# Kernel tuning notes

Measured on AMD Instinct MI355X. Metric: run time of the kernel, lower is better.

The kernel has to match this reference:

```python
import jax, jax.numpy as jnp
import numpy as np

D_IN = 128
HID = 32
HEADS = 8
OUT = 16
N = 50000
E = 400000
NEG_SLOPE = 0.2


def setup_inputs() -> dict:
    key = jax.random.key(0)
    ks = jax.random.split(key, 12)
    s = lambda k, sh: jax.random.normal(k, sh, dtype=jnp.float32) * 0.05
    return {
        "x": jax.random.normal(ks[0], (N, D_IN), dtype=jnp.float32),
        "edge_index": jax.random.randint(ks[1], (2, E), 0, N, dtype=jnp.int64),
        # conv_1: GATv2, heads=8, concat=True
        "W1l": s(ks[2], (D_IN, HEADS * HID)),
        "W1r": s(ks[3], (D_IN, HEADS * HID)),
        "att1": s(ks[4], (HEADS, HID)),
        "b1": jnp.zeros((HEADS * HID,), dtype=jnp.float32),
        # conv_2: GATv2, heads=1, concat=False
        "W2l": s(ks[5], (HEADS * HID, HID)),
        "W2r": s(ks[6], (HEADS * HID, HID)),
        "att2": s(ks[7], (1, HID)),
        "b2": jnp.zeros((HID,), dtype=jnp.float32),
        # final linear
        "Wlin": s(ks[8], (HID, OUT)),
        "blin": jnp.zeros((OUT,), dtype=jnp.float32),
    }


def _gatv2(x, src, dst, Wl, Wr, att, bias, n_nodes):
    heads, ch = att.shape
    xl = (x @ Wl).reshape(n_nodes, heads, ch)   # source-side transform
    xr = (x @ Wr).reshape(n_nodes, heads, ch)   # target-side transform
    # per-edge GATv2 score: a^T leaky_relu(xl_i + xr_j)
    e = jax.nn.leaky_relu(xl[src] + xr[dst], NEG_SLOPE)        # [E,H,C]
    logits = jnp.einsum('ehc,hc->eh', e, att)                  # [E,H]
    # segment softmax grouped by destination node
    m = jax.ops.segment_max(logits, dst, num_segments=n_nodes)
    m = jnp.where(jnp.isfinite(m), m, 0.0)
    p = jnp.exp(logits - m[dst])
    denom = jax.ops.segment_sum(p, dst, num_segments=n_nodes)
    alpha = p / jnp.maximum(denom[dst], 1e-16)                 # [E,H]
    # scatter-sum aggregation of weighted source features
    out = jax.ops.segment_sum(alpha[:, :, None] * xl[src], dst, num_segments=n_nodes)
    return out + bias.reshape(1, heads, ch)                    # [N,H,C]


def reference(x, edge_index, W1l, W1r, att1, b1, W2l, W2r, att2, b2, Wlin, blin):
    n = x.shape[0]
    loops = jnp.arange(n, dtype=edge_index.dtype)
    ei = jnp.concatenate([edge_index, jnp.stack([loops, loops])], axis=1)  # add_self_loops=True
    src, dst = ei[0], ei[1]

    h = _gatv2(x, src, dst, W1l, W1r, att1, b1, n)   # [N,8,32]
    h = jax.nn.elu(h.reshape(n, -1))                  # concat=True; dropout=identity (eval)

    h = _gatv2(h, src, dst, W2l, W2r, att2, b2, n)   # [N,1,32]
    h = jax.nn.elu(h[:, 0, :])                        # concat=False, heads=1 -> mean == squeeze

    return h @ Wlin + blin                            # [N,16]
```

## Files before the change

### kernel.cpp

```cpp
#include <hip/hip_runtime.h>
#include <cstdint>
#include <cstddef>

#define N_NODES 50000
#define N_EDGES 400000
#define E_TOT   (N_EDGES + N_NODES)
#define D_INF   128
#define C1      256
#define HIDC    32
#define OUTC    16
#define NEG_SLOPE 0.2f
#define LOG2E   1.44269504088896340736f

#define ESRC_CAP (E_TOT + 3 * N_NODES + 16)

#define ZB_DEG ((N_NODES + 255) / 256)
#define TB_W   ((2 * D_INF * C1 + 2 * C1 * HIDC + 255) / 256)
#define PREP_GRID (ZB_DEG + TB_W + 1)

#define GB1   ((((N_NODES + 31) / 32) + 3) / 4)
#define DEGB  ((E_TOT + 255) / 256)
#define FILLB ((E_TOT + 255) / 256)

typedef __bf16 bf16x8 __attribute__((ext_vector_type(8)));
typedef float  floatx4 __attribute__((ext_vector_type(4)));
typedef float  floatx2 __attribute__((ext_vector_type(2)));
typedef int    intx4  __attribute__((ext_vector_type(4)));
typedef unsigned int uintx4 __attribute__((ext_vector_type(4)));
typedef unsigned int uintx2 __attribute__((ext_vector_type(2)));
typedef unsigned short ushortx8 __attribute__((ext_vector_type(8)));
typedef unsigned short ushortx4 __attribute__((ext_vector_type(4)));

__device__ __forceinline__ unsigned short f2bf(float f) {
  unsigned int u = __builtin_bit_cast(unsigned int, f);
  u += 0x7FFFu + ((u >> 16) & 1u);
  return (unsigned short)(u >> 16);
}
__device__ __forceinline__ float bf2f(unsigned short u) {
  return __builtin_bit_cast(float, (unsigned int)u << 16);
}
__device__ __forceinline__ floatx2 bf2x2(unsigned int u) {
  floatx2 r;
  r.x = __builtin_bit_cast(float, u << 16);
  r.y = __builtin_bit_cast(float, u & 0xffff0000u);
  return r;
}

__device__ __forceinline__ int ld_src(const int* ei, int f, int e) {
  return f ? ei[2 * e] : ei[e];
}
__device__ __forceinline__ int ld_dst(const int* ei, int f, int e) {
  return f ? ei[2 * (N_EDGES + e)] : ei[N_EDGES + e];
}

__global__ __launch_bounds__(256) void k_prep(
    const int* __restrict__ ei,
    const float* __restrict__ W1l, const float* __restrict__ W1r,
    const float* __restrict__ W2l, const float* __restrict__ W2r,
    unsigned short* __restrict__ W1lT, unsigned short* __restrict__ W1rT,
    unsigned short* __restrict__ W2lT, unsigned short* __restrict__ W2rT,
    int* __restrict__ deg, int* __restrict__ total, int* __restrict__ flag) {
  __shared__ int sdet;
  const int bid = blockIdx.x;
  const int tid = threadIdx.x;
  if (bid < ZB_DEG) {
    const int i = bid * 256 + tid;
    if (i < N_NODES) deg[i] = 0;
    if (bid == 0 && tid == 0) *total = 0;
    return;
  }
  if (bid < ZB_DEG + TB_W) {
    int idx = (bid - ZB_DEG) * 256 + tid;
    if (idx < D_INF * C1) {
      const int r = idx >> 8, c = idx & 255;
      W1lT[c * D_INF + r] = f2bf(W1l[idx]);
    } else if (idx < 2 * D_INF * C1) {
      idx -= D_INF * C1;
      const int r = idx >> 8, c = idx & 255;
      W1rT[c * D_INF + r] = f2bf(W1r[idx]);
    } else if (idx < 2 * D_INF * C1 + C1 * HIDC) {
      idx -= 2 * D_INF * C1;
      const int r = idx >> 5, c = idx & 31;
      W2lT[c * C1 + r] = f2bf(W2l[idx]);
    } else {
      idx -= 2 * D_INF * C1 + C1 * HIDC;
      const int r = idx >> 5, c = idx & 31;
      W2rT[c * C1 + r] = f2bf(W2r[idx]);
    }
    return;
  }
  if (tid == 0) sdet = 0;
  __syncthreads();
  if (tid < 64) atomicOr(&sdet, ei[2 * tid + 1]);
  __syncthreads();
  if (tid == 0) *flag = (sdet == 0) ? 1 : 0;
}

__global__ __launch_bounds__(256) void k_alloc(
    const int* __restrict__ deg, int* __restrict__ rowptr,
    int* __restrict__ cursor, int* __restrict__ total) {
  const int i = blockIdx.x * 256 + threadIdx.x;
  const int lane = threadIdx.x & 63;
  const int d  = (i < N_NODES) ? deg[i] : 0;
  const int d4 = (d + 3) & ~3;
  int incl = d4;
#pragma unroll
  for (int off = 1; off < 64; off <<= 1) {
    int t = __shfl_up(incl, off);
    if (lane >= off) incl += t;
  }
  const int wtot = __shfl(incl, 63);
  int wb = 0;
  if (lane == 63) wb = atomicAdd(total, wtot);
  wb = __shfl(wb, 63);
  if (i < N_NODES) {
    const int e = wb + incl - d4;
    rowptr[i] = e;
    cursor[i] = e;
  }
}

__global__ void k_fill(const int* __restrict__ ei, const int* __restrict__ flag,
                       int* __restrict__ cursor, int* __restrict__ esrc) {
  int e = blockIdx.x * 256 + threadIdx.x;
  if (e < E_TOT) {
    int src, dst;
    if (e < N_EDGES) { src = ld_src(ei, *flag, e); dst = ld_dst(ei, *flag, e); }
    else             { src = dst = e - N_EDGES; }
    if ((unsigned)src < N_NODES && (unsigned)dst < N_NODES) {
      int pos = atomicAdd(&cursor[dst], 1);
      esrc[pos] = src;
    }
  }
}

__device__ __forceinline__ bf16x8 load8(const unsigned short* p) {
  uintx4 raw = *reinterpret_cast<const uintx4*>(p);
  return __builtin_bit_cast(bf16x8, raw);
}
__device__ __forceinline__ bf16x8 load8(const float* p) {
  floatx4 a = *reinterpret_cast<const floatx4*>(p);
  floatx4 b = *reinterpret_cast<const floatx4*>(p + 4);
  ushortx8 u;
#pragma unroll
  for (int i = 0; i < 4; ++i) { u[i] = f2bf(a[i]); u[4 + i] = f2bf(b[i]); }
  return __builtin_bit_cast(bf16x8, u);
}

template <int K, int NCOLS, typename AT>
__device__ __forceinline__ void gemm_dual_body(
    int unit, int lane, const AT* __restrict__ A,
    const unsigned short* __restrict__ BT0, const unsigned short* __restrict__ BT1,
    unsigned short* __restrict__ C0, unsigned short* __restrict__ C1_, int M) {
  const int lo = lane & 15;
  const int q  = lane >> 4;
  const int r0 = unit * 32;
  if (r0 >= M) return;
  const bool two = (r0 + 16) < M;
  constexpr int KB = K / 32;

  bf16x8 afrag[2][KB];
#pragma unroll
  for (int kb = 0; kb < KB; ++kb)
    afrag[0][kb] = load8(A + (size_t)(r0 + lo) * K + kb * 32 + q * 8);
  if (two) {
#pragma unroll
    for (int kb = 0; kb < KB; ++kb)
      afrag[1][kb] = load8(A + (size_t)(r0 + 16 + lo) * K + kb * 32 + q * 8);
  }

#pragma unroll
  for (int o = 0; o < 2; ++o) {
    const unsigned short* BT = o ? BT1 : BT0;
    unsigned short* C = o ? C1_ : C0;
#pragma unroll
    for (int nt = 0; nt < NCOLS / 16; ++nt) {
      floatx4 acc0 = {0.f, 0.f, 0.f, 0.f};
      floatx4 acc1 = {0.f, 0.f, 0.f, 0.f};
      const unsigned short* bptr = BT + (size_t)(nt * 16 + lo) * K + q * 8;
#pragma unroll
      for (int kb = 0; kb < KB; ++kb) {
        bf16x8 b = load8(bptr + kb * 32);
        acc0 = __builtin_amdgcn_mfma_f32_16x16x32_bf16(afrag[0][kb], b, acc0, 0, 0, 0);
        if (two)
          acc1 = __builtin_amdgcn_mfma_f32_16x16x32_bf16(afrag[1][kb], b, acc1, 0, 0, 0);
      }
#pragma unroll
      for (int r = 0; r < 4; ++r) {
        C[(size_t)(r0 + q * 4 + r) * NCOLS + nt * 16 + lo] = f2bf(acc0[r]);
        if (two)
          C[(size_t)(r0 + 16 + q * 4 + r) * NCOLS + nt * 16 + lo] = f2bf(acc1[r]);
      }
    }
  }
}

__global__ __launch_bounds__(256) void k_gemm1_deg(
    const float* __restrict__ A,
    const unsigned short* __restrict__ BT0, const unsigned short* __restrict__ BT1,
    unsigned short* __restrict__ C0, unsigned short* __restrict__ C1_,
    const int* __restrict__ ei, const int* __restrict__ flag,
    int* __restrict__ deg) {
  if (blockIdx.x < GB1) {
    const int wave = threadIdx.x >> 6;
    const int lane = threadIdx.x & 63;
    gemm_dual_body<D_INF, C1, float>(blockIdx.x * 4 + wave, lane,
                                     A, BT0, BT1, C0, C1_, N_NODES);
    return;
  }
  const int e = (blockIdx.x - GB1) * 256 + threadIdx.x;
  if (e < E_TOT) {
    int dst = (e < N_EDGES) ? ld_dst(ei, *flag, e) : (e - N_EDGES);
    if ((unsigned)dst < N_NODES) atomicAdd(&deg[dst], 1);
  }
}

__global__ __launch_bounds__(256) void k_gemm2(
    const unsigned short* __restrict__ A,
    const unsigned short* __restrict__ BT0, const unsigned short* __restrict__ BT1,
    unsigned short* __restrict__ C0, unsigned short* __restrict__ C1_) {
  const int wave = threadIdx.x >> 6;
  const int lane = threadIdx.x & 63;
  gemm_dual_body<C1, HIDC, unsigned short>(blockIdx.x * 4 + wave, lane,
                                           A, BT0, BT1, C0, C1_, N_NODES);
}

__global__ __launch_bounds__(256) void k_gat1(
    const unsigned short* __restrict__ xl1, const unsigned short* __restrict__ xr1,
    const float* __restrict__ att1, const float* __restrict__ b1,
    const int* __restrict__ rowptr, const int* __restrict__ deg,
    const int* __restrict__ esrc, unsigned short* __restrict__ h1) {
  const int wave = threadIdx.x >> 6;
  const int lane = threadIdx.x & 63;
  const int dst = blockIdx.x * 4 + wave;
  if (dst >= N_NODES) return;
  const int h = lane >> 5;
  const int w = lane & 31;
  const int cb = w * 8;
  const unsigned short* __restrict__ xb = xl1 + cb;

  const int beg = rowptr[dst];
  const int n   = deg[dst];
  const int* __restrict__ ep = esrc + beg;

  floatx2 xr2v[4], att2v[4];
  {
    uintx4 r = *reinterpret_cast<const uintx4*>(xr1 + (size_t)dst * C1 + cb);
    floatx4 a0 = *reinterpret_cast<const floatx4*>(att1 + cb);
    floatx4 a1 = *reinterpret_cast<const floatx4*>(att1 + cb + 4);
#pragma unroll
    for (int j = 0; j < 4; ++j) xr2v[j] = bf2x2(r[j]);
    att2v[0] = floatx2{a0.x, a0.y} * LOG2E;
    att2v[1] = floatx2{a0.z, a0.w} * LOG2E;
    att2v[2] = floatx2{a1.x, a1.y} * LOG2E;
    att2v[3] = floatx2{a1.z, a1.w} * LOG2E;
  }

  float l = 0.f;
  floatx2 acc2[4] = {{0.f, 0.f}, {0.f, 0.f}, {0.f, 0.f}, {0.f, 0.f}};

  auto gath = [&](int a, int b) {
    const int s = h ? b : a;
    return *reinterpret_cast<const uintx4*>(xb + (size_t)s * C1);
  };
  auto process = [&](uintx4 cur, float keep) {
    floatx2 xs2[4];
    floatx2 v2 = {0.f, 0.f};
#pragma unroll
    for (int j = 0; j < 4; ++j) {
      xs2[j] = bf2x2(cur[j]);
      floatx2 s2 = xs2[j] + xr2v[j];
      floatx2 e2 = __builtin_elementwise_max(s2, s2 * NEG_SLOPE);
      v2 = __builtin_elementwise_fma(e2, att2v[j], v2);
    }
    float v = v2.x + v2.y;
    v += __shfl_xor(v, 1);
    v += __shfl_xor(v, 2);
    v = __builtin_amdgcn_fmed3f(v, -100.f, 100.f);
    const float p = __builtin_amdgcn_exp2f(v) * keep;
    l += p;
    const floatx2 p2 = {p, p};
#pragma unroll
    for (int j = 0; j < 4; ++j)
      acc2[j] = __builtin_elementwise_fma(p2, xs2[j], acc2[j]);
  };

  intx4 ja = *reinterpret_cast<const intx4*>(ep);
  uintx4 g0 = {0u,0u,0u,0u}, g1 = {0u,0u,0u,0u};
  if (h     < n) g0 = gath(ja.x, ja.y);
  if (h + 2 < n) g1 = gath(ja.z, ja.w);
  intx4 jb4 = *reinterpret_cast<const intx4*>(ep + 4);
  uintx4 t0 = {0u,0u,0u,0u}, t1 = {0u,0u,0u,0u};
  if (n > 4) {
    const int r1 = n - 4;
    if (h     < r1) t0 = gath(jb4.x, jb4.y);
    if (h + 2 < r1) t1 = gath(jb4.z, jb4.w);
  }
  intx4 jn = *reinterpret_cast<const intx4*>(ep + 8);

  int base = 0;
  while (true) {
    const int rem = n - base;
    uintx4 u0 = {0u,0u,0u,0u}, u1 = {0u,0u,0u,0u};
    if (rem > 8) {
      const int r2 = rem - 8;
      if (h     < r2) u0 = gath(jn.x, jn.y);
      if (h + 2 < r2) u1 = gath(jn.z, jn.w);
      jn = *reinterpret_cast<const intx4*>(ep + base + 12);
    }
    if (rem >= 4) {
      process(g0, 1.f);
      process(g1, 1.f);
    } else {
      process(g0, (h     < rem) ? 1.f : 0.f);
      process(g1, (h + 2 < rem) ? 1.f : 0.f);
    }
    if (rem <= 4) break;
    g0 = t0; g1 = t1; t0 = u0; t1 = u1;
    base += 4;
  }

  l += __shfl_xor(l, 32);
#pragma unroll
  for (int j = 0; j < 4; ++j) {
    acc2[j].x += __shfl_xor(acc2[j].x, 32);
    acc2[j].y += __shfl_xor(acc2[j].y, 32);
  }

  if (h == 0) {
    const float inv = 1.f / fmaxf(l, 1e-16f);
    ushortx8 ob;
#pragma unroll
    for (int j = 0; j < 4; ++j) {
      float z0 = acc2[j].x * inv + b1[cb + 2 * j];
      float z1 = acc2[j].y * inv + b1[cb + 2 * j + 1];
      z0 = z0 > 0.f ? z0 : (__expf(z0) - 1.f);
      z1 = z1 > 0.f ? z1 : (__expf(z1) - 1.f);
      ob[2 * j]     = f2bf(z0);
      ob[2 * j + 1] = f2bf(z1);
    }
    *reinterpret_cast<ushortx8*>(h1 + (size_t)dst * C1 + cb) = ob;
  }
}

__global__ __launch_bounds__(256) void k_gat2(
    const unsigned short* __restrict__ xl2, const unsigned short* __restrict__ xr2,
    const float* __restrict__ att2, const float* __restrict__ b2,
    const float* __restrict__ Wlin, const float* __restrict__ blin,
    const int* __restrict__ rowptr, const int* __restrict__ deg,
    const int* __restrict__ esrc, float* __restrict__ out) {
  __shared__ float sh[4][32];
  const int wave = threadIdx.x >> 6;
  const int lane = threadIdx.x & 63;
  const int dst = blockIdx.x * 4 + wave;
  if (dst >= N_NODES) return;
  const int o8 = lane >> 3;
  const int w = lane & 7;
  const int cb = w * 4;

  floatx2 xr2v[2], att2v[2];
  {
    uintx2 r = *reinterpret_cast<const uintx2*>(xr2 + (size_t)dst * HIDC + cb);
    floatx4 a = *reinterpret_cast<const floatx4*>(att2 + cb);
    xr2v[0] = bf2x2(r[0]);
    xr2v[1] = bf2x2(r[1]);
    att2v[0] = floatx2{a.x, a.y} * LOG2E;
    att2v[1] = floatx2{a.z, a.w} * LOG2E;
  }

  const int beg = rowptr[dst];
  const int n   = deg[dst];
  const int* __restrict__ ep = esrc + beg;

  float l = 0.f;
  floatx2 acc2[2] = {{0.f, 0.f}, {0.f, 0.f}};

  auto process = [&](uintx2 cur) {
    floatx2 xs2[2];
    floatx2 v2 = {0.f, 0.f};
#pragma unroll
    for (int j = 0; j < 2; ++j) {
      xs2[j] = bf2x2(cur[j]);
      floatx2 s2 = xs2[j] + xr2v[j];
      floatx2 e2 = __builtin_elementwise_max(s2, s2 * NEG_SLOPE);
      v2 = __builtin_elementwise_fma(e2, att2v[j], v2);
    }
    float v = v2.x + v2.y;
    v += __shfl_xor(v, 1);
    v += __shfl_xor(v, 2);
    v += __shfl_xor(v, 4);
    v = __builtin_amdgcn_fmed3f(v, -100.f, 100.f);
    const float p = __builtin_amdgcn_exp2f(v);
    l += p;
    const floatx2 p2 = {p, p};
#pragma unroll
    for (int j = 0; j < 2; ++j)
      acc2[j] = __builtin_elementwise_fma(p2, xs2[j], acc2[j]);
  };

  uintx2 bufa = {0u, 0u}, bufb = {0u, 0u};
  if (o8 < n)
    bufa = *reinterpret_cast<const uintx2*>(xl2 + (size_t)ep[o8] * HIDC + cb);
  if (o8 + 8 < n)
    bufb = *reinterpret_cast<const uintx2*>(xl2 + (size_t)ep[o8 + 8] * HIDC + cb);
  int i = o8;
  while (i < n) {
    process(bufa);
    if (i + 16 < n)
      bufa = *reinterpret_cast<const uintx2*>(xl2 + (size_t)ep[i + 16] * HIDC + cb);
    i += 8;
    if (i >= n) break;
    process(bufb);
    if (i + 16 < n)
      bufb = *reinterpret_cast<const uintx2*>(xl2 + (size_t)ep[i + 16] * HIDC + cb);
    i += 8;
  }

#pragma unroll
  for (int k = 8; k < 64; k <<= 1) {
    l += __shfl_xor(l, k);
#pragma unroll
    for (int j = 0; j < 2; ++j) {
      acc2[j].x += __shfl_xor(acc2[j].x, k);
      acc2[j].y += __shfl_xor(acc2[j].y, k);
    }
  }

  if (o8 == 0) {
    const float inv = 1.f / fmaxf(l, 1e-16f);
#pragma unroll
    for (int j = 0; j < 2; ++j) {
      float z0 = acc2[j].x * inv + b2[cb + 2 * j];
      float z1 = acc2[j].y * inv + b2[cb + 2 * j + 1];
      z0 = z0 > 0.f ? z0 : (__expf(z0) - 1.f);
      z1 = z1 > 0.f ? z1 : (__expf(z1) - 1.f);
      sh[wave][cb + 2 * j]     = z0;
      sh[wave][cb + 2 * j + 1] = z1;
    }
  }
  if (lane < OUTC) {
    float o = blin[lane];
#pragma unroll
    for (int k = 0; k < 32; ++k)
      o = fmaf(sh[wave][k], Wlin[k * OUTC + lane], o);
    out[(size_t)dst * OUTC + lane] = o;
  }
}

static inline int cdiv(int a, int b) { return (a + b - 1) / b; }

extern "C" void kernel_launch(void* const* d_in, const int* in_sizes, int n_in,
                              void* d_out, int out_size, void* d_ws, size_t ws_size,
                              hipStream_t stream) {
  const float* x    = (const float*)d_in[0];
  const int*   ei   = (const int*)d_in[1];
  const float* W1l  = (const float*)d_in[2];
  const float* W1r  = (const float*)d_in[3];
  const float* att1 = (const float*)d_in[4];
  const float* b1   = (const float*)d_in[5];
  const float* W2l  = (const float*)d_in[6];
  const float* W2r  = (const float*)d_in[7];
  const float* att2 = (const float*)d_in[8];
  const float* b2   = (const float*)d_in[9];
  const float* Wlin = (const float*)d_in[10];
  const float* blin = (const float*)d_in[11];
  float* out = (float*)d_out;

  char* w = (char*)d_ws;
  auto alloc = [&](size_t bytes) -> char* {
    char* p = w;
    w += (bytes + 255) & ~(size_t)255;
    return p;
  };
  char* regionA = alloc((size_t)N_NODES * C1 * 2);
  unsigned short* xl1 = (unsigned short*)regionA;
  unsigned short* xl2 = (unsigned short*)regionA;
  unsigned short* xr2 = (unsigned short*)(regionA + (size_t)N_NODES * HIDC * 2 + 256);
  unsigned short* xr1 = (unsigned short*)alloc((size_t)N_NODES * C1 * 2);
  unsigned short* h1  = xr1;
  unsigned short* W1lT = (unsigned short*)alloc((size_t)D_INF * C1 * 2);
  unsigned short* W1rT = (unsigned short*)alloc((size_t)D_INF * C1 * 2);
  unsigned short* W2lT = (unsigned short*)alloc((size_t)C1 * HIDC * 2);
  unsigned short* W2rT = (unsigned short*)alloc((size_t)C1 * HIDC * 2);
  int* rowptr = (int*)alloc((size_t)N_NODES * 4);
  int* cursor = (int*)alloc((size_t)N_NODES * 4);
  int* deg    = (int*)alloc((size_t)N_NODES * 4);
  int* esrc   = (int*)alloc((size_t)ESRC_CAP * 4);
  int* flag   = (int*)alloc(4);
  int* total  = (int*)alloc(4);

  k_prep<<<PREP_GRID, 256, 0, stream>>>(ei, W1l, W1r, W2l, W2r,
                                        W1lT, W1rT, W2lT, W2rT,
                                        deg, total, flag);

  k_gemm1_deg<<<GB1 + DEGB, 256, 0, stream>>>(x, W1lT, W1rT, xl1, xr1,
                                              ei, flag, deg);

  k_alloc<<<cdiv(N_NODES, 256), 256, 0, stream>>>(deg, rowptr, cursor, total);
  k_fill<<<FILLB, 256, 0, stream>>>(ei, flag, cursor, esrc);

  k_gat1<<<cdiv(N_NODES, 4), 256, 0, stream>>>(xl1, xr1, att1, b1,
                                               rowptr, deg, esrc, h1);

  k_gemm2<<<cdiv(cdiv(N_NODES, 32), 4), 256, 0, stream>>>(h1, W2lT, W2rT, xl2, xr2);

  k_gat2<<<cdiv(N_NODES, 4), 256, 0, stream>>>(xl2, xr2, att2, b2, Wlin, blin,
                                               rowptr, deg, esrc, out);
}
```

Measured before the change: 272.8 us.

## Reorder graph-build stages, overlap GEMM1 with CSR fill, split dual GEMM waves

Degree counting moves into the weight-prep kernel, which now runs after a memset and a separate flag-detect kernel. The first GEMM is fused with the CSR fill kernel rather than the degree kernel, so the fill's atomics overlap the matmul. Each GEMM wave now computes one output matrix instead of both, doubling wave count and cutting per-wave work for better occupancy and load balance, at the cost of loading each A tile twice. The GAT1 gather loop is simplified to a two-buffer prefetch of per-edge indices, dropping vectorized index loads and the masked tail handling.

```diff
diff --git a/kernel.cpp b/kernel.cpp
--- a/kernel.cpp
+++ b/kernel.cpp
@@ -14,18 +14,17 @@
 
 #define ESRC_CAP (E_TOT + 3 * N_NODES + 16)
 
-#define ZB_DEG ((N_NODES + 255) / 256)
 #define TB_W   ((2 * D_INF * C1 + 2 * C1 * HIDC + 255) / 256)
-#define PREP_GRID (ZB_DEG + TB_W + 1)
-
-#define GB1   ((((N_NODES + 31) / 32) + 3) / 4)
-#define DEGB  ((E_TOT + 255) / 256)
-#define FILLB ((E_TOT + 255) / 256)
+#define DEGB   ((E_TOT + 255) / 256)
+#define FILLB  ((E_TOT + 255) / 256)
+
+#define UNITS1 ((N_NODES + 31) / 32)
+#define GB1S   ((2 * UNITS1 + 3) / 4)
+#define GB2S   ((2 * UNITS1 + 3) / 4)
 
 typedef __bf16 bf16x8 __attribute__((ext_vector_type(8)));
 typedef float  floatx4 __attribute__((ext_vector_type(4)));
 typedef float  floatx2 __attribute__((ext_vector_type(2)));
-typedef int    intx4  __attribute__((ext_vector_type(4)));
 typedef unsigned int uintx4 __attribute__((ext_vector_type(4)));
 typedef unsigned int uintx2 __attribute__((ext_vector_type(2)));
 typedef unsigned short ushortx8 __attribute__((ext_vector_type(8)));
@@ -53,47 +52,49 @@
   return f ? ei[2 * (N_EDGES + e)] : ei[N_EDGES + e];
 }
 
+__global__ void k_detect(const int* __restrict__ ei, int* __restrict__ flag) {
+  __shared__ int s;
+  if (threadIdx.x == 0) s = 0;
+  __syncthreads();
+  atomicOr(&s, ei[2 * threadIdx.x + 1]);
+  __syncthreads();
+  if (threadIdx.x == 0) *flag = (s == 0) ? 1 : 0;
+}
+
 __global__ __launch_bounds__(256) void k_prep(
-    const int* __restrict__ ei,
+    const int* __restrict__ ei, const int* __restrict__ flag,
     const float* __restrict__ W1l, const float* __restrict__ W1r,
     const float* __restrict__ W2l, const float* __restrict__ W2r,
     unsigned short* __restrict__ W1lT, unsigned short* __restrict__ W1rT,
     unsigned short* __restrict__ W2lT, unsigned short* __restrict__ W2rT,
-    int* __restrict__ deg, int* __restrict__ total, int* __restrict__ flag) {
-  __shared__ int sdet;
+    int* __restrict__ deg) {
   const int bid = blockIdx.x;
   const int tid = threadIdx.x;
-  if (bid < ZB_DEG) {
-    const int i = bid * 256 + tid;
-    if (i < N_NODES) deg[i] = 0;
-    if (bid == 0 && tid == 0) *total = 0;
+  if (bid < DEGB) {
+    const int e = bid * 256 + tid;
+    if (e < E_TOT) {
+      int dst = (e < N_EDGES) ? ld_dst(ei, *flag, e) : (e - N_EDGES);
+      if ((unsigned)dst < N_NODES) atomicAdd(&deg[dst], 1);
+    }
     return;
   }
-  if (bid < ZB_DEG + TB_W) {
-    int idx = (bid - ZB_DEG) * 256 + tid;
-    if (idx < D_INF * C1) {
-      const int r = idx >> 8, c = idx & 255;
-      W1lT[c * D_INF + r] = f2bf(W1l[idx]);
-    } else if (idx < 2 * D_INF * C1) {
-      idx -= D_INF * C1;
-      const int r = idx >> 8, c = idx & 255;
-      W1rT[c * D_INF + r] = f2bf(W1r[idx]);
-    } else if (idx < 2 * D_INF * C1 + C1 * HIDC) {
-      idx -= 2 * D_INF * C1;
-      const int r = idx >> 5, c = idx & 31;
-      W2lT[c * C1 + r] = f2bf(W2l[idx]);
-    } else {
-      idx -= 2 * D_INF * C1 + C1 * HIDC;
-      const int r = idx >> 5, c = idx & 31;
-      W2rT[c * C1 + r] = f2bf(W2r[idx]);
-    }
-    return;
-  }
-  if (tid == 0) sdet = 0;
-  __syncthreads();
-  if (tid < 64) atomicOr(&sdet, ei[2 * tid + 1]);
-  __syncthreads();
-  if (tid == 0) *flag = (sdet == 0) ? 1 : 0;
+  int idx = (bid - DEGB) * 256 + tid;
+  if (idx < D_INF * C1) {
+    const int r = idx >> 8, c = idx & 255;
+    W1lT[c * D_INF + r] = f2bf(W1l[idx]);
+  } else if (idx < 2 * D_INF * C1) {
+    idx -= D_INF * C1;
+    const int r = idx >> 8, c = idx & 255;
+    W1rT[c * D_INF + r] = f2bf(W1r[idx]);
+  } else if (idx < 2 * D_INF * C1 + C1 * HIDC) {
+    idx -= 2 * D_INF * C1;
+    const int r = idx >> 5, c = idx & 31;
+    W2lT[c * C1 + r] = f2bf(W2l[idx]);
+  } else if (idx < 2 * (D_INF * C1 + C1 * HIDC)) {
+    idx -= 2 * D_INF * C1 + C1 * HIDC;
+    const int r = idx >> 5, c = idx & 31;
+    W2rT[c * C1 + r] = f2bf(W2r[idx]);
+  }
 }
 
 __global__ __launch_bounds__(256) void k_alloc(
@@ -120,9 +121,78 @@
   }
 }
 
-__global__ void k_fill(const int* __restrict__ ei, const int* __restrict__ flag,
-                       int* __restrict__ cursor, int* __restrict__ esrc) {
-  int e = blockIdx.x * 256 + threadIdx.x;
+__device__ __forceinline__ bf16x8 load8(const unsigned short* p) {
+  uintx4 raw = *reinterpret_cast<const uintx4*>(p);
+  return __builtin_bit_cast(bf16x8, raw);
+}
+__device__ __forceinline__ bf16x8 load8(const float* p) {
+  floatx4 a = *reinterpret_cast<const floatx4*>(p);
+  floatx4 b = *reinterpret_cast<const floatx4*>(p + 4);
+  ushortx8 u;
+#pragma unroll
+  for (int i = 0; i < 4; ++i) { u[i] = f2bf(a[i]); u[4 + i] = f2bf(b[i]); }
+  return __builtin_bit_cast(bf16x8, u);
+}
+
+template <int K, int NCOLS, typename AT>
+__device__ __forceinline__ void gemm_body(
+    int unit, int lane, const AT* __restrict__ A,
+    const unsigned short* __restrict__ BT,
+    unsigned short* __restrict__ C, int M) {
+  const int lo = lane & 15;
+  const int q  = lane >> 4;
+  const int r0 = unit * 32;
+  if (r0 >= M) return;
+  const bool two = (r0 + 16) < M;
+  constexpr int KB = K / 32;
+
+  bf16x8 afrag[2][KB];
+#pragma unroll
+  for (int kb = 0; kb < KB; ++kb)
+    afrag[0][kb] = load8(A + (size_t)(r0 + lo) * K + kb * 32 + q * 8);
+  if (two) {
+#pragma unroll
+    for (int kb = 0; kb < KB; ++kb)
+      afrag[1][kb] = load8(A + (size_t)(r0 + 16 + lo) * K + kb * 32 + q * 8);
+  }
+
+#pragma unroll
+  for (int nt = 0; nt < NCOLS / 16; ++nt) {
+    floatx4 acc0 = {0.f, 0.f, 0.f, 0.f};
+    floatx4 acc1 = {0.f, 0.f, 0.f, 0.f};
+    const unsigned short* bptr = BT + (size_t)(nt * 16 + lo) * K + q * 8;
+#pragma unroll
+    for (int kb = 0; kb < KB; ++kb) {
+      bf16x8 b = load8(bptr + kb * 32);
+      acc0 = __builtin_amdgcn_mfma_f32_16x16x32_bf16(afrag[0][kb], b, acc0, 0, 0, 0);
+      if (two)
+        acc1 = __builtin_amdgcn_mfma_f32_16x16x32_bf16(afrag[1][kb], b, acc1, 0, 0, 0);
+    }
+#pragma unroll
+    for (int r = 0; r < 4; ++r) {
+      C[(size_t)(r0 + q * 4 + r) * NCOLS + nt * 16 + lo] = f2bf(acc0[r]);
+      if (two)
+        C[(size_t)(r0 + 16 + q * 4 + r) * NCOLS + nt * 16 + lo] = f2bf(acc1[r]);
+    }
+  }
+}
+
+__global__ __launch_bounds__(256) void k_gemm1_fill(
+    const float* __restrict__ A,
+    const unsigned short* __restrict__ BT0, const unsigned short* __restrict__ BT1,
+    unsigned short* __restrict__ C0, unsigned short* __restrict__ C1_,
+    const int* __restrict__ ei, const int* __restrict__ flag,
+    int* __restrict__ cursor, int* __restrict__ esrc) {
+  if (blockIdx.x < GB1S) {
+    const int wave = threadIdx.x >> 6;
+    const int lane = threadIdx.x & 63;
+    const int unit = blockIdx.x * 4 + wave;
+    const int o = (unit >= UNITS1) ? 1 : 0;
+    const int ru = unit - o * UNITS1;
+    gemm_body<D_INF, C1, float>(ru, lane, A, o ? BT1 : BT0, o ? C1_ : C0, N_NODES);
+    return;
+  }
+  const int e = (blockIdx.x - GB1S) * 256 + threadIdx.x;
   if (e < E_TOT) {
     int src, dst;
     if (e < N_EDGES) { src = ld_src(ei, *flag, e); dst = ld_dst(ei, *flag, e); }
@@ -134,95 +204,16 @@
   }
 }
 
-__device__ __forceinline__ bf16x8 load8(const unsigned short* p) {
-  uintx4 raw = *reinterpret_cast<const uintx4*>(p);
-  return __builtin_bit_cast(bf16x8, raw);
-}
-__device__ __forceinline__ bf16x8 load8(const float* p) {
-  floatx4 a = *reinterpret_cast<const floatx4*>(p);
-  floatx4 b = *reinterpret_cast<const floatx4*>(p + 4);
-  ushortx8 u;
-#pragma unroll
-  for (int i = 0; i < 4; ++i) { u[i] = f2bf(a[i]); u[4 + i] = f2bf(b[i]); }
-  return __builtin_bit_cast(bf16x8, u);
-}
-
-template <int K, int NCOLS, typename AT>
-__device__ __forceinline__ void gemm_dual_body(
-    int unit, int lane, const AT* __restrict__ A,
-    const unsigned short* __restrict__ BT0, const unsigned short* __restrict__ BT1,
-    unsigned short* __restrict__ C0, unsigned short* __restrict__ C1_, int M) {
-  const int lo = lane & 15;
-  const int q  = lane >> 4;
-  const int r0 = unit * 32;
-  if (r0 >= M) return;
-  const bool two = (r0 + 16) < M;
-  constexpr int KB = K / 32;
-
-  bf16x8 afrag[2][KB];
-#pragma unroll
-  for (int kb = 0; kb < KB; ++kb)
-    afrag[0][kb] = load8(A + (size_t)(r0 + lo) * K + kb * 32 + q * 8);
-  if (two) {
-#pragma unroll
-    for (int kb = 0; kb < KB; ++kb)
-      afrag[1][kb] = load8(A + (size_t)(r0 + 16 + lo) * K + kb * 32 + q * 8);
-  }
-
-#pragma unroll
-  for (int o = 0; o < 2; ++o) {
-    const unsigned short* BT = o ? BT1 : BT0;
-    unsigned short* C = o ? C1_ : C0;
-#pragma unroll
-    for (int nt = 0; nt < NCOLS / 16; ++nt) {
-      floatx4 acc0 = {0.f, 0.f, 0.f, 0.f};
-      floatx4 acc1 = {0.f, 0.f, 0.f, 0.f};
-      const unsigned short* bptr = BT + (size_t)(nt * 16 + lo) * K + q * 8;
-#pragma unroll
-      for (int kb = 0; kb < KB; ++kb) {
-        bf16x8 b = load8(bptr + kb * 32);
-        acc0 = __builtin_amdgcn_mfma_f32_16x16x32_bf16(afrag[0][kb], b, acc0, 0, 0, 0);
-        if (two)
-          acc1 = __builtin_amdgcn_mfma_f32_16x16x32_bf16(afrag[1][kb], b, acc1, 0, 0, 0);
-      }
-#pragma unroll
-      for (int r = 0; r < 4; ++r) {
-        C[(size_t)(r0 + q * 4 + r) * NCOLS + nt * 16 + lo] = f2bf(acc0[r]);
-        if (two)
-          C[(size_t)(r0 + 16 + q * 4 + r) * NCOLS + nt * 16 + lo] = f2bf(acc1[r]);
-      }
-    }
-  }
-}
-
-__global__ __launch_bounds__(256) void k_gemm1_deg(
-    const float* __restrict__ A,
-    const unsigned short* __restrict__ BT0, const unsigned short* __restrict__ BT1,
-    unsigned short* __restrict__ C0, unsigned short* __restrict__ C1_,
-    const int* __restrict__ ei, const int* __restrict__ flag,
-    int* __restrict__ deg) {
-  if (blockIdx.x < GB1) {
-    const int wave = threadIdx.x >> 6;
-    const int lane = threadIdx.x & 63;
-    gemm_dual_body<D_INF, C1, float>(blockIdx.x * 4 + wave, lane,
-                                     A, BT0, BT1, C0, C1_, N_NODES);
-    return;
-  }
-  const int e = (blockIdx.x - GB1) * 256 + threadIdx.x;
-  if (e < E_TOT) {
-    int dst = (e < N_EDGES) ? ld_dst(ei, *flag, e) : (e - N_EDGES);
-    if ((unsigned)dst < N_NODES) atomicAdd(&deg[dst], 1);
-  }
-}
-
 __global__ __launch_bounds__(256) void k_gemm2(
     const unsigned short* __restrict__ A,
     const unsigned short* __restrict__ BT0, const unsigned short* __restrict__ BT1,
     unsigned short* __restrict__ C0, unsigned short* __restrict__ C1_) {
   const int wave = threadIdx.x >> 6;
   const int lane = threadIdx.x & 63;
-  gemm_dual_body<C1, HIDC, unsigned short>(blockIdx.x * 4 + wave, lane,
-                                           A, BT0, BT1, C0, C1_, N_NODES);
+  const int unit = blockIdx.x * 4 + wave;
+  const int o = (unit >= UNITS1) ? 1 : 0;
+  const int ru = unit - o * UNITS1;
+  gemm_body<C1, HIDC, unsigned short>(ru, lane, A, o ? BT1 : BT0, o ? C1_ : C0, N_NODES);
 }
 
 __global__ __launch_bounds__(256) void k_gat1(
@@ -237,11 +228,6 @@
   const int h = lane >> 5;
   const int w = lane & 31;
   const int cb = w * 8;
-  const unsigned short* __restrict__ xb = xl1 + cb;
-
-  const int beg = rowptr[dst];
-  const int n   = deg[dst];
-  const int* __restrict__ ep = esrc + beg;
 
   floatx2 xr2v[4], att2v[4];
   {
@@ -256,14 +242,14 @@
     att2v[3] = floatx2{a1.z, a1.w} * LOG2E;
   }
 
+  const int beg = rowptr[dst];
+  const int n   = deg[dst];
+  const int* __restrict__ ep = esrc + beg;
+
   float l = 0.f;
   floatx2 acc2[4] = {{0.f, 0.f}, {0.f, 0.f}, {0.f, 0.f}, {0.f, 0.f}};
 
-  auto gath = [&](int a, int b) {
-    const int s = h ? b : a;
-    return *reinterpret_cast<const uintx4*>(xb + (size_t)s * C1);
-  };
-  auto process = [&](uintx4 cur, float keep) {
+  auto process = [&](uintx4 cur) {
     floatx2 xs2[4];
     floatx2 v2 = {0.f, 0.f};
 #pragma unroll
@@ -276,8 +262,8 @@
     float v = v2.x + v2.y;
     v += __shfl_xor(v, 1);
     v += __shfl_xor(v, 2);
-    v = __builtin_amdgcn_fmed3f(v, -100.f, 100.f);
-    const float p = __builtin_amdgcn_exp2f(v) * keep;
+    v = fminf(fmaxf(v, -100.f), 100.f);
+    const float p = __builtin_amdgcn_exp2f(v);
     l += p;
     const floatx2 p2 = {p, p};
 #pragma unroll
@@ -285,39 +271,22 @@
       acc2[j] = __builtin_elementwise_fma(p2, xs2[j], acc2[j]);
   };
 
-  intx4 ja = *reinterpret_cast<const intx4*>(ep);
-  uintx4 g0 = {0u,0u,0u,0u}, g1 = {0u,0u,0u,0u};
-  if (h     < n) g0 = gath(ja.x, ja.y);
-  if (h + 2 < n) g1 = gath(ja.z, ja.w);
-  intx4 jb4 = *reinterpret_cast<const intx4*>(ep + 4);
-  uintx4 t0 = {0u,0u,0u,0u}, t1 = {0u,0u,0u,0u};
-  if (n > 4) {
-    const int r1 = n - 4;
-    if (h     < r1) t0 = gath(jb4.x, jb4.y);
-    if (h + 2 < r1) t1 = gath(jb4.z, jb4.w);
-  }
-  intx4 jn = *reinterpret_cast<const intx4*>(ep + 8);
-
-  int base = 0;
-  while (true) {
-    const int rem = n - base;
-    uintx4 u0 = {0u,0u,0u,0u}, u1 = {0u,0u,0u,0u};
-    if (rem > 8) {
-      const int r2 = rem - 8;
-      if (h     < r2) u0 = gath(jn.x, jn.y);
-      if (h + 2 < r2) u1 = gath(jn.z, jn.w);
-      jn = *reinterpret_cast<const intx4*>(ep + base + 12);
-    }
-    if (rem >= 4) {
-      process(g0, 1.f);
-      process(g1, 1.f);
-    } else {
-      process(g0, (h     < rem) ? 1.f : 0.f);
-      process(g1, (h + 2 < rem) ? 1.f : 0.f);
-    }
-    if (rem <= 4) break;
-    g0 = t0; g1 = t1; t0 = u0; t1 = u1;
-    base += 4;
+  uintx4 bufa = {0u, 0u, 0u, 0u}, bufb = {0u, 0u, 0u, 0u};
+  if (h < n)
+    bufa = *reinterpret_cast<const uintx4*>(xl1 + (size_t)ep[h] * C1 + cb);
+  if (h + 2 < n)
+    bufb = *reinterpret_cast<const uintx4*>(xl1 + (size_t)ep[h + 2] * C1 + cb);
+  int i = h;
+  while (i < n) {
+    process(bufa);
+    if (i + 4 < n)
+      bufa = *reinterpret_cast<const uintx4*>(xl1 + (size_t)ep[i + 4] * C1 + cb);
+    i += 2;
+    if (i >= n) break;
+    process(bufb);
+    if (i + 4 < n)
+      bufb = *reinterpret_cast<const uintx4*>(xl1 + (size_t)ep[i + 4] * C1 + cb);
+    i += 2;
   }
 
   l += __shfl_xor(l, 32);
@@ -389,7 +358,7 @@
     v += __shfl_xor(v, 1);
     v += __shfl_xor(v, 2);
     v += __shfl_xor(v, 4);
-    v = __builtin_amdgcn_fmed3f(v, -100.f, 100.f);
+    v = fminf(fmaxf(v, -100.f), 100.f);
     const float p = __builtin_amdgcn_exp2f(v);
     l += p;
     const floatx2 p2 = {p, p};
@@ -484,25 +453,26 @@
   unsigned short* W2rT = (unsigned short*)alloc((size_t)C1 * HIDC * 2);
   int* rowptr = (int*)alloc((size_t)N_NODES * 4);
   int* cursor = (int*)alloc((size_t)N_NODES * 4);
-  int* deg    = (int*)alloc((size_t)N_NODES * 4);
+  int* deg    = (int*)alloc((size_t)(N_NODES + 1) * 4);
+  int* total  = deg + N_NODES;
   int* esrc   = (int*)alloc((size_t)ESRC_CAP * 4);
   int* flag   = (int*)alloc(4);
-  int* total  = (int*)alloc(4);
-
-  k_prep<<<PREP_GRID, 256, 0, stream>>>(ei, W1l, W1r, W2l, W2r,
-                                        W1lT, W1rT, W2lT, W2rT,
-                                        deg, total, flag);
-
-  k_gemm1_deg<<<GB1 + DEGB, 256, 0, stream>>>(x, W1lT, W1rT, xl1, xr1,
-                                              ei, flag, deg);
+
+  hipMemsetAsync(deg, 0, (size_t)(N_NODES + 1) * 4, stream);
+  k_detect<<<1, 64, 0, stream>>>(ei, flag);
+
+  k_prep<<<DEGB + TB_W, 256, 0, stream>>>(ei, flag, W1l, W1r, W2l, W2r,
+                                          W1lT, W1rT, W2lT, W2rT, deg);
 
   k_alloc<<<cdiv(N_NODES, 256), 256, 0, stream>>>(deg, rowptr, cursor, total);
-  k_fill<<<FILLB, 256, 0, stream>>>(ei, flag, cursor, esrc);
+
+  k_gemm1_fill<<<GB1S + FILLB, 256, 0, stream>>>(x, W1lT, W1rT, xl1, xr1,
+                                                 ei, flag, cursor, esrc);
 
   k_gat1<<<cdiv(N_NODES, 4), 256, 0, stream>>>(xl1, xr1, att1, b1,
                                                rowptr, deg, esrc, h1);
 
-  k_gemm2<<<cdiv(cdiv(N_NODES, 32), 4), 256, 0, stream>>>(h1, W2lT, W2rT, xl2, xr2);
+  k_gemm2<<<GB2S, 256, 0, stream>>>(h1, W2lT, W2rT, xl2, xr2);
 
   k_gat2<<<cdiv(N_NODES, 4), 256, 0, stream>>>(xl2, xr2, att2, b2, Wlin, blin,
                                                rowptr, deg, esrc, out);
```

New measurement: 270.6 us. Within noise of the previous version (-0.8%).
